# Performance work log

Measured on AMD Instinct MI355X. Metric: run time of the kernel, lower is better.

The kernel has to match this reference:

```python
import jax, jax.numpy as jnp
import numpy as np

N_NODES = 50000
N_EDGES = 100000
NUM_GRAPHS = 1024
EMB = 600
NUM_ATOMIC = 119      # Num_atomic_number
NUM_HYB = 8           # HybridizationType values
NUM_AROM = 2
NUM_CHIR = 4          # ChiralType values
NUM_CHARGE = 9
NUM_BOND_TYPE = 22    # BondType values


def setup_inputs() -> dict:
    key = jax.random.key(0)
    ks = jax.random.split(key, 20)
    # integer graph data
    atom = jnp.stack([
        jax.random.randint(ks[0], (N_NODES,), 0, NUM_ATOMIC),
        jax.random.randint(ks[1], (N_NODES,), 0, NUM_HYB),
        jax.random.randint(ks[2], (N_NODES,), 0, NUM_AROM),
        jax.random.randint(ks[3], (N_NODES,), 0, NUM_CHIR),
        jax.random.randint(ks[4], (N_NODES,), 0, NUM_CHARGE),
    ], axis=1)
    bond_index = jax.random.randint(ks[5], (2, N_EDGES), 0, N_NODES)
    bond_attr = jnp.stack([
        jax.random.randint(ks[6], (N_EDGES,), 0, NUM_BOND_TYPE),
        jax.random.randint(ks[7], (N_EDGES,), 0, NUM_ATOMIC),
    ], axis=1)
    batch = jnp.sort(jax.random.randint(ks[8], (N_NODES,), 0, NUM_GRAPHS))
    # parameters (kaiming-uniform-ish scale)
    def emb(k, n, d):
        bound = float(np.sqrt(6.0 / d))
        return jax.random.uniform(k, (n, d), minval=-bound, maxval=bound, dtype=jnp.float32)
    def lin(k, out_d, in_d):
        bound = float(np.sqrt(6.0 / in_d))
        return jax.random.uniform(k, (out_d, in_d), minval=-bound, maxval=bound, dtype=jnp.float32)
    return {
        "atom": atom, "bond_index": bond_index, "bond_attr": bond_attr, "batch": batch,
        "W_atom_num": emb(ks[9], NUM_ATOMIC, EMB),
        "W_hyb": emb(ks[10], NUM_HYB, EMB),
        "W_arom": emb(ks[11], NUM_AROM, EMB),
        "W_chir": emb(ks[12], NUM_CHIR, EMB),
        "W_charge": emb(ks[13], NUM_CHARGE, EMB),
        "W_bond_type": emb(ks[14], NUM_BOND_TYPE, EMB),
        "W_bond_atom_i": emb(ks[15], NUM_ATOMIC, EMB),
        "W_sl_atom": emb(ks[16], NUM_ATOMIC, EMB),
        "W_sl": emb(ks[17], 1, EMB),
        "W1": lin(ks[18], EMB, EMB), "b1": jnp.zeros((EMB,), jnp.float32),
        "W2": lin(ks[19], EMB // 2, EMB), "b2": jnp.zeros((EMB // 2,), jnp.float32),
        "W3": lin(jax.random.fold_in(key, 99), 1, EMB // 2),
    }


def reference(atom, bond_index, bond_attr, batch,
              W_atom_num, W_hyb, W_arom, W_chir, W_charge,
              W_bond_type, W_bond_atom_i, W_sl_atom, W_sl,
              W1, b1, W2, b2, W3):
    N = atom.shape[0]
    # Step 1: node embedding = sum of 5 lookups  [N, EMB]
    node = (W_atom_num[atom[:, 0]] + W_hyb[atom[:, 1]] + W_arom[atom[:, 2]]
            + W_chir[atom[:, 3]] + W_charge[atom[:, 4]])
    # Step 2: edge embeddings; self-loops appended after real bonds
    bond_emb = W_bond_type[bond_attr[:, 0]] + W_bond_atom_i[bond_attr[:, 1]]  # [E, EMB]
    sl_emb = W_sl_atom[atom[:, 0]] + W_sl[0]                                  # [N, EMB]
    edge_emb = jnp.concatenate([bond_emb, sl_emb], axis=0)                    # [E+N, EMB]
    loop = jnp.arange(N, dtype=bond_index.dtype)
    src = jnp.concatenate([bond_index[0], loop])
    dst = jnp.concatenate([bond_index[1], loop])
    # Step 3: 2 message-passing layers: gather src, multiply edge_emb, scatter-add to dst
    for _ in range(2):
        node = jax.ops.segment_sum(node[src] * edge_emb, dst, num_segments=N)
    # Step 4: energy MLP  ReLU -> Linear(d,d) -> ReLU -> Linear(d,d/2) -> ReLU -> Linear(d/2,1)
    h = jax.nn.relu(node)
    h = jax.nn.relu(h @ W1.T + b1)
    h = jax.nn.relu(h @ W2.T + b2)
    node_energy = h @ W3.T  # [N, 1]
    # Step 5: global add pool per graph
    dg = jax.ops.segment_sum(node_energy, batch, num_segments=NUM_GRAPHS)  # [NUM_GRAPHS, 1]
    return dg
```

## Files before the change

kernel.cpp:

```cpp
#include <hip/hip_runtime.h>

#define EMB 600
#define Q4  150
#define KP  608

typedef unsigned short ushortT;
typedef __attribute__((ext_vector_type(8))) short short8;
typedef __attribute__((ext_vector_type(4))) short short4v;
typedef __attribute__((ext_vector_type(4))) float f32x4;

__device__ __forceinline__ float4 f4add(float4 a, float4 b) {
    return make_float4(a.x + b.x, a.y + b.y, a.z + b.z, a.w + b.w);
}
__device__ __forceinline__ float4 f4fma(float4 acc, float4 v, float4 e) {
    return make_float4(fmaf(v.x, e.x, acc.x), fmaf(v.y, e.y, acc.y),
                       fmaf(v.z, e.z, acc.z), fmaf(v.w, e.w, acc.w));
}
__device__ __forceinline__ ushortT bf16_rne(float x) {
    unsigned u = __float_as_uint(x);
    return (ushortT)((u + 0x7fffu + ((u >> 16) & 1u)) >> 16);
}
__device__ __forceinline__ float bf16_to_f(ushortT h) {
    return __uint_as_float(((unsigned)h) << 16);
}
__device__ __forceinline__ short4v f4_to_bf4(float4 v) {
    short4v r;
    r[0] = (short)bf16_rne(v.x);
    r[1] = (short)bf16_rne(v.y);
    r[2] = (short)bf16_rne(v.z);
    r[3] = (short)bf16_rne(v.w);
    return r;
}
__device__ __forceinline__ float4 bf4_to_f4(short4v h) {
    return make_float4(bf16_to_f((ushortT)h[0]), bf16_to_f((ushortT)h[1]),
                       bf16_to_f((ushortT)h[2]), bf16_to_f((ushortT)h[3]));
}

__device__ __forceinline__ size_t frag_off(int row, int col) {
    return ((size_t)((row >> 4) * 19 + (col >> 5)) * 64
            + (row & 15) + 16 * ((col >> 3) & 3)) * 8 + (col & 7);
}

__global__ void k_node_embed(const int* __restrict__ atom,
                             const float4* __restrict__ Wa,
                             const float4* __restrict__ Wh,
                             const float4* __restrict__ War,
                             const float4* __restrict__ Wc,
                             const float4* __restrict__ Wch,
                             float4* __restrict__ out, int N) {
    int idx = blockIdx.x * blockDim.x + threadIdx.x;
    int total = N * Q4;
    if (idx >= total) return;
    int n = idx / Q4;
    int q = idx - n * Q4;
    const int* a = atom + n * 5;
    float4 r = Wa[a[0] * Q4 + q];
    r = f4add(r, Wh [a[1] * Q4 + q]);
    r = f4add(r, War[a[2] * Q4 + q]);
    r = f4add(r, Wc [a[3] * Q4 + q]);
    r = f4add(r, Wch[a[4] * Q4 + q]);
    out[idx] = r;
}

__global__ void k_hist(const int* __restrict__ bdst, int* __restrict__ counts, int E) {
    int i = blockIdx.x * blockDim.x + threadIdx.x;
    if (i < E) atomicAdd(&counts[bdst[i]], 1);
}

__global__ __launch_bounds__(256) void k_scan_l1(const int* __restrict__ counts,
                                                 int* __restrict__ offsets,
                                                 int* __restrict__ blocksums, int N) {
    __shared__ int s[256];
    int t = threadIdx.x;
    int i = blockIdx.x * 256 + t;
    int v = (i < N) ? counts[i] : 0;
    s[t] = v;
    __syncthreads();
#pragma unroll
    for (int off = 1; off < 256; off <<= 1) {
        int x = (t >= off) ? s[t - off] : 0;
        __syncthreads();
        s[t] += x;
        __syncthreads();
    }
    if (i < N) offsets[i] = s[t] - v;
    if (t == 255) blocksums[blockIdx.x] = s[255];
}

__global__ __launch_bounds__(256) void k_scan_l2(int* __restrict__ blocksums,
                                                 int* __restrict__ blockpref, int nb) {
    __shared__ int s[256];
    int t = threadIdx.x;
    int v = (t < nb) ? blocksums[t] : 0;
    s[t] = v;
    __syncthreads();
#pragma unroll
    for (int off = 1; off < 256; off <<= 1) {
        int x = (t >= off) ? s[t - off] : 0;
        __syncthreads();
        s[t] += x;
        __syncthreads();
    }
    if (t < nb) blockpref[t] = s[t] - v;
}

__global__ __launch_bounds__(256) void k_scan_l3(int* __restrict__ offsets,
                                                 int* __restrict__ cursor,
                                                 const int* __restrict__ blockpref, int N) {
    int i = blockIdx.x * 256 + threadIdx.x;
    if (i < N) {
        int o = offsets[i] + blockpref[blockIdx.x];
        offsets[i] = o;
        cursor[i]  = o;
    }
}

__global__ void k_scatter(const int* __restrict__ bdst, int* __restrict__ cursor,
                          int* __restrict__ edge_list, int E) {
    int i = blockIdx.x * blockDim.x + threadIdx.x;
    if (i < E) {
        int pos = atomicAdd(&cursor[bdst[i]], 1);
        edge_list[pos] = i;
    }
}

__global__ __launch_bounds__(256) void k_mp_gather_b(
        const int* __restrict__ bsrc, const int* __restrict__ battr,
        const int* __restrict__ atom,
        const int* __restrict__ offsets, const int* __restrict__ counts,
        const int* __restrict__ edge_list,
        const float4* __restrict__ Wbt, const float4* __restrict__ Wbai,
        const float4* __restrict__ Wsla, const float4* __restrict__ Wsl,
        const float4* __restrict__ in, ushortT* __restrict__ out, int N) {
    int wid  = (int)((blockIdx.x * blockDim.x + threadIdx.x) >> 6);
    int lane = threadIdx.x & 63;
    int d    = wid >> 1;
    int half = wid & 1;
    if (d >= N) return;
    int q1 = 75 * half + lane;
    int q2 = q1 + 64;
    bool has2 = lane < 11;

    int start = offsets[d], cnt = counts[d];
    int s = 0, t0 = 0, t1 = 0;
    if (cnt > 0) {
        int eid = edge_list[start];
        s  = bsrc[eid];
        t0 = battr[eid * 2 + 0];
        t1 = battr[eid * 2 + 1];
    }

    const float4* slA = Wsla + atom[d * 5] * Q4;
    const float4* inr = in + (size_t)d * Q4;
    float4 acc1 = make_float4(0, 0, 0, 0), acc2 = acc1;
    acc1 = f4fma(acc1, inr[q1], f4add(slA[q1], Wsl[q1]));
    if (has2) acc2 = f4fma(acc2, inr[q2], f4add(slA[q2], Wsl[q2]));

    for (int k = 0; k < cnt; k++) {
        int ns = s, nt0 = t0, nt1 = t1;
        if (k + 1 < cnt) {
            int ne = edge_list[start + k + 1];
            ns  = bsrc[ne];
            nt0 = battr[ne * 2 + 0];
            nt1 = battr[ne * 2 + 1];
        }
        const float4* e0 = Wbt  + t0 * Q4;
        const float4* e1 = Wbai + t1 * Q4;
        const float4* sr = in + (size_t)s * Q4;
        acc1 = f4fma(acc1, sr[q1], f4add(e0[q1], e1[q1]));
        if (has2) acc2 = f4fma(acc2, sr[q2], f4add(e0[q2], e1[q2]));
        s = ns; t0 = nt0; t1 = nt1;
    }
    ushortT* orow = out + (size_t)d * EMB;
    *(short4v*)(orow + q1 * 4) = f4_to_bf4(acc1);
    if (has2) *(short4v*)(orow + q2 * 4) = f4_to_bf4(acc2);
}

__device__ __forceinline__ void frag_store4h(ushortT* __restrict__ hi,
                                             int d, int q, float4 v) {
    int kc = q >> 3, ks = (q >> 1) & 3, halfw = q & 1;
    size_t off = ((size_t)((d >> 4) * 19 + kc) * 64 + (d & 15) + 16 * ks) * 8
                 + halfw * 4;
    float vv[4] = {v.x, v.y, v.z, v.w};
    short4v h4;
#pragma unroll
    for (int j = 0; j < 4; j++)
        h4[j] = (short)bf16_rne(fmaxf(vv[j], 0.f));
    *(short4v*)(hi + off) = h4;
}

__global__ __launch_bounds__(256) void k_mp_gather_rs(
        const int* __restrict__ bsrc, const int* __restrict__ battr,
        const int* __restrict__ atom,
        const int* __restrict__ offsets, const int* __restrict__ counts,
        const int* __restrict__ edge_list,
        const float4* __restrict__ Wbt, const float4* __restrict__ Wbai,
        const float4* __restrict__ Wsla, const float4* __restrict__ Wsl,
        const ushortT* __restrict__ in,
        ushortT* __restrict__ hi, int N) {
    int wid  = (int)((blockIdx.x * blockDim.x + threadIdx.x) >> 6);
    int lane = threadIdx.x & 63;
    int d    = wid >> 1;
    int half = wid & 1;
    if (d >= N) return;
    int q1 = 75 * half + lane;
    int q2 = q1 + 64;
    bool has2 = lane < 11;

    int start = offsets[d], cnt = counts[d];
    int s = 0, t0 = 0, t1 = 0;
    if (cnt > 0) {
        int eid = edge_list[start];
        s  = bsrc[eid];
        t0 = battr[eid * 2 + 0];
        t1 = battr[eid * 2 + 1];
    }

    const float4* slA = Wsla + atom[d * 5] * Q4;
    const ushortT* inr = in + (size_t)d * EMB;
    float4 acc1 = make_float4(0, 0, 0, 0), acc2 = acc1;
    acc1 = f4fma(acc1, bf4_to_f4(*(const short4v*)(inr + q1 * 4)),
                 f4add(slA[q1], Wsl[q1]));
    if (has2) acc2 = f4fma(acc2, bf4_to_f4(*(const short4v*)(inr + q2 * 4)),
                           f4add(slA[q2], Wsl[q2]));

    for (int k = 0; k < cnt; k++) {
        int ns = s, nt0 = t0, nt1 = t1;
        if (k + 1 < cnt) {
            int ne = edge_list[start + k + 1];
            ns  = bsrc[ne];
            nt0 = battr[ne * 2 + 0];
            nt1 = battr[ne * 2 + 1];
        }
        const float4* e0 = Wbt  + t0 * Q4;
        const float4* e1 = Wbai + t1 * Q4;
        const ushortT* sr = in + (size_t)s * EMB;
        acc1 = f4fma(acc1, bf4_to_f4(*(const short4v*)(sr + q1 * 4)),
                     f4add(e0[q1], e1[q1]));
        if (has2) acc2 = f4fma(acc2, bf4_to_f4(*(const short4v*)(sr + q2 * 4)),
                               f4add(e0[q2], e1[q2]));
        s = ns; t0 = nt0; t1 = nt1;
    }
    frag_store4h(hi, d, q1, acc1);
    if (has2) frag_store4h(hi, d, q2, acc2);
    if (half == 0 && lane == 31) {
        size_t off = ((size_t)((d >> 4) * 19 + 18) * 64 + (d & 15) + 48) * 8;
        short8 z = {0, 0, 0, 0, 0, 0, 0, 0};
        *(short8*)(hi + off) = z;
    }
}

__global__ void k_split_w_frag(const float* __restrict__ src,
                               short8* __restrict__ dst,
                               int rows_in, int cb_count) {
    int idx = blockIdx.x * blockDim.x + threadIdx.x;
    int total = cb_count * 19 * 64;
    if (idx >= total) return;
    int lane = idx & 63;
    int tile = idx >> 6;
    int cb = tile / 19, kc = tile - cb * 19;
    int col = cb * 16 + (lane & 15);
    int k0  = kc * 32 + (lane >> 4) * 8;
    short8 h;
#pragma unroll
    for (int j = 0; j < 8; j++) {
        int k = k0 + j;
        float x = (col < rows_in && k < 600) ? src[(size_t)col * 600 + k] : 0.f;
        h[j] = (short)bf16_rne(x);
    }
    dst[idx] = h;
}

struct FragSet { short8 a[4], b[4]; };

__device__ __forceinline__ void frag_load(FragSet& f,
        const short8* __restrict__ Af, const short8* __restrict__ Bf,
        int aBase, int bBase, int kc) {
    int ak = aBase + kc * 64;
    int bk = bBase + kc * 64;
#pragma unroll
    for (int i = 0; i < 4; i++) {
        f.a[i] = Af[ak + i * 1216];
        f.b[i] = Bf[bk + i * 1216];
    }
}

__device__ __forceinline__ void frag_mfma(const FragSet& f, f32x4 acc[4][4]) {
#pragma unroll
    for (int i = 0; i < 4; i++)
#pragma unroll
        for (int j = 0; j < 4; j++)
            acc[i][j] = __builtin_amdgcn_mfma_f32_16x16x32_bf16(f.a[i], f.b[j], acc[i][j], 0, 0, 0);
}

__device__ __forceinline__ void gemm_core_reg(
        const short8* __restrict__ Af, const short8* __restrict__ Bf,
        int aBase, int bBase, f32x4 acc[4][4]) {
    for (int kc = 0; kc < 19; kc++) {
        FragSet f;
        frag_load(f, Af, Bf, aBase, bBase, kc);
        frag_mfma(f, acc);
    }
}

__device__ __forceinline__ void decode_wg(int ncb, int& rowblk, int& colblk) {
    int nwg  = gridDim.x;
    int orig = blockIdx.x;
    int q = nwg >> 3, r = nwg & 7;
    int xcd = orig & 7, rank = orig >> 3;
    int wgid = (xcd < r ? xcd * (q + 1) : r * (q + 1) + (xcd - r) * q) + rank;
    rowblk = wgid / ncb;
    colblk = wgid - rowblk * ncb;
}

__global__ __launch_bounds__(256, 4) void k_gemm1r(
        const short8* __restrict__ Af, const short8* __restrict__ Wf,
        const float* __restrict__ b1,
        ushortT* __restrict__ Hf, int N) {
    int rowblk, colblk;
    decode_wg(5, rowblk, colblk);
    int row0 = rowblk * 128;
    int col0 = colblk * 128;
    int t = threadIdx.x, w = t >> 6, l = t & 63;
    int wr = w >> 1, wc = w & 1, fr = l & 15, fq = l >> 4;

    int aBase = (rowblk * 8 + wr * 4) * 1216 + l;
    int bBase = (colblk * 8 + wc * 4) * 1216 + l;
    f32x4 acc[4][4];
#pragma unroll
    for (int i = 0; i < 4; i++)
#pragma unroll
        for (int j = 0; j < 4; j++) acc[i][j] = f32x4{0.f, 0.f, 0.f, 0.f};
    gemm_core_reg(Af, Wf, aBase, bBase, acc);

#pragma unroll
    for (int i = 0; i < 4; i++) {
#pragma unroll
        for (int j = 0; j < 4; j++) {
            int col = col0 + wc * 64 + j * 16 + fr;
            float bias = (col < 600) ? b1[col] : 0.f;
#pragma unroll
            for (int r = 0; r < 4; r++) {
                int row = row0 + wr * 64 + i * 16 + fq * 4 + r;
                if (row >= N) continue;
                if (col < 600) {
                    float x = fmaxf(acc[i][j][r] + bias, 0.f);
                    Hf[frag_off(row, col)] = bf16_rne(x);
                } else if (col < KP) {
                    Hf[frag_off(row, col)] = 0;
                }
            }
        }
    }
}

__global__ __launch_bounds__(256, 4) void k_gemm2r(
        const short8* __restrict__ Af, const short8* __restrict__ Wf,
        const float* __restrict__ b2, const float* __restrict__ W3,
        float* __restrict__ energy, int N) {
    __shared__ float sE[128];
    int rowblk, colblk;
    decode_wg(3, rowblk, colblk);
    int row0 = rowblk * 128;
    int col0 = colblk * 128;
    int t = threadIdx.x, w = t >> 6, l = t & 63;
    int wr = w >> 1, wc = w & 1, fr = l & 15, fq = l >> 4;

    int aBase = (rowblk * 8 + wr * 4) * 1216 + l;
    int bBase = (colblk * 8 + wc * 4) * 1216 + l;
    f32x4 acc[4][4];
#pragma unroll
    for (int i = 0; i < 4; i++)
#pragma unroll
        for (int j = 0; j < 4; j++) acc[i][j] = f32x4{0.f, 0.f, 0.f, 0.f};
    gemm_core_reg(Af, Wf, aBase, bBase, acc);

    if (t < 128) sE[t] = 0.f;
    __syncthreads();
#pragma unroll
    for (int i = 0; i < 4; i++) {
        float p[4] = {0.f, 0.f, 0.f, 0.f};
#pragma unroll
        for (int j = 0; j < 4; j++) {
            int col = col0 + wc * 64 + j * 16 + fr;
            if (col < 300) {
                float bias = b2[col];
                float wv   = W3[col];
#pragma unroll
                for (int r = 0; r < 4; r++)
                    p[r] += fmaxf(acc[i][j][r] + bias, 0.f) * wv;
            }
        }
#pragma unroll
        for (int r = 0; r < 4; r++) {
            float v = p[r];
            v += __shfl_xor(v, 1, 64);
            v += __shfl_xor(v, 2, 64);
            v += __shfl_xor(v, 4, 64);
            v += __shfl_xor(v, 8, 64);
            p[r] = v;
        }
        if (fr == 0) {
#pragma unroll
            for (int r = 0; r < 4; r++)
                atomicAdd(&sE[wr * 64 + i * 16 + fq * 4 + r], p[r]);
        }
    }
    __syncthreads();
    if (t < 128) {
        int row = row0 + t;
        if (row < N) atomicAdd(&energy[row], sE[t]);
    }
}

__global__ void k_pool(const float* __restrict__ energy, const int* __restrict__ batch,
                       float* __restrict__ dg, int N) {
    int i = blockIdx.x * blockDim.x + threadIdx.x;
    int lane = threadIdx.x & 63;
    float v = (i < N) ? energy[i] : 0.f;
    int   b = (i < N) ? batch[i]  : -1;
#pragma unroll
    for (int off = 1; off < 64; off <<= 1) {
        float vv = __shfl_down(v, off, 64);
        int   bb = __shfl_down(b, off, 64);
        if (lane + off < 64 && bb == b) v += vv;
    }
    int pb = __shfl_up(b, 1, 64);
    if (i < N && (lane == 0 || pb != b)) atomicAdd(&dg[b], v);
}

extern "C" void kernel_launch(void* const* d_in, const int* in_sizes, int n_in,
                              void* d_out, int out_size, void* d_ws, size_t ws_size,
                              hipStream_t stream) {
    const int* atom       = (const int*)d_in[0];
    const int* bond_index = (const int*)d_in[1];
    const int* bond_attr  = (const int*)d_in[2];
    const int* batch      = (const int*)d_in[3];
    const float* Wa   = (const float*)d_in[4];
    const float* Wh   = (const float*)d_in[5];
    const float* War  = (const float*)d_in[6];
    const float* Wc   = (const float*)d_in[7];
    const float* Wch  = (const float*)d_in[8];
    const float* Wbt  = (const float*)d_in[9];
    const float* Wbai = (const float*)d_in[10];
    const float* Wsla = (const float*)d_in[11];
    const float* Wsl  = (const float*)d_in[12];
    const float* W1   = (const float*)d_in[13];
    const float* b1   = (const float*)d_in[14];
    const float* W2   = (const float*)d_in[15];
    const float* b2   = (const float*)d_in[16];
    const float* W3   = (const float*)d_in[17];

    int N = in_sizes[0] / 5;
    int E = in_sizes[1] / 2;
    int Mb = (N + 127) / 128;
    int Npad = Mb * 128;
    int nTiles = Npad / 16;
    int nb = (N + 255) / 256;

    size_t regionBytes = (size_t)Npad * KP * 4;
    char* base = (char*)d_ws;
    float* nodeA = (float*)base;
    ushortT* nodeBh = (ushortT*)(base + regionBytes);
    short8* Af = (short8*)nodeA;
    short8* Hf = (short8*)nodeBh;
    char* tail = base + 2 * regionBytes;
    float* energy  = (float*)tail;
    int* counts    = (int*)(energy + N);
    int* offsets   = counts + N;
    int* cursor    = offsets + N;
    int* edge_list = cursor + N;
    short8* W1f    = (short8*)(edge_list + E);
    short8* W2f    = W1f + 40 * 19 * 64;
    int* blocksums = (int*)(W2f + 24 * 19 * 64);
    int* blockpref = blocksums + 256;

    const int* bsrc = bond_index;
    const int* bdst = bond_index + E;

    hipMemsetAsync(counts, 0, (size_t)N * sizeof(int), stream);
    k_hist<<<(E + 255) / 256, 256, 0, stream>>>(bdst, counts, E);
    k_scan_l1<<<nb, 256, 0, stream>>>(counts, offsets, blocksums, N);
    k_scan_l2<<<1, 256, 0, stream>>>(blocksums, blockpref, nb);
    k_scan_l3<<<nb, 256, 0, stream>>>(offsets, cursor, blockpref, N);
    k_scatter<<<(E + 255) / 256, 256, 0, stream>>>(bdst, cursor, edge_list, E);

    k_split_w_frag<<<(40 * 19 * 64 + 255) / 256, 256, 0, stream>>>(W1, W1f, 600, 40);
    k_split_w_frag<<<(24 * 19 * 64 + 255) / 256, 256, 0, stream>>>(W2, W2f, 300, 24);

    {
        int total = N * Q4;
        k_node_embed<<<(total + 255) / 256, 256, 0, stream>>>(
            atom, (const float4*)Wa, (const float4*)Wh, (const float4*)War,
            (const float4*)Wc, (const float4*)Wch, (float4*)nodeA, N);
    }

    int mpblocks = (2 * N * 64 + 255) / 256;
    k_mp_gather_b<<<mpblocks, 256, 0, stream>>>(bsrc, bond_attr, atom,
        offsets, counts, edge_list,
        (const float4*)Wbt, (const float4*)Wbai, (const float4*)Wsla, (const float4*)Wsl,
        (const float4*)nodeA, nodeBh, N);

    {
        int firstPad = N / 16;
        size_t offB  = (size_t)firstPad * 1216 * 16;
        size_t cntB  = (size_t)(nTiles - firstPad) * 1216 * 16;
        if (cntB) hipMemsetAsync((char*)Af + offB, 0, cntB, stream);
    }

    k_mp_gather_rs<<<mpblocks, 256, 0, stream>>>(bsrc, bond_attr, atom,
        offsets, counts, edge_list,
        (const float4*)Wbt, (const float4*)Wbai, (const float4*)Wsla, (const float4*)Wsl,
        nodeBh, (ushortT*)Af, N);

    k_gemm1r<<<Mb * 5, 256, 0, stream>>>(Af, W1f, b1, (ushortT*)Hf, N);

    hipMemsetAsync(energy, 0, (size_t)N * sizeof(float), stream);
    k_gemm2r<<<Mb * 3, 256, 0, stream>>>(Hf, W2f, b2, W3, energy, N);

    hipMemsetAsync(d_out, 0, (size_t)out_size * sizeof(float), stream);
    k_pool<<<(N + 255) / 256, 256, 0, stream>>>(energy, batch, (float*)d_out, N);
}
```

Before: 348.9 us.

## Store initial node embeddings as bf16 and double-buffer edge gathers in message passing

The initial node embedding is now written in bf16 rather than fp32, which halves the bytes written by the embed kernel and read by the first message-passing layer. Both message-passing kernels share a new loop that fetches the source row and edge weights one edge ahead and the edge indices two edges ahead, so memory latency overlaps with the FMA work. The price is extra registers per thread and bf16 rounding of the layer-1 input, which slightly changes numerics.

Result: slower. 358.2 us (+2.7%).

```diff
diff --git a/kernel.cpp b/kernel.cpp
--- a/kernel.cpp
+++ b/kernel.cpp
@@ -41,13 +41,13 @@
             + (row & 15) + 16 * ((col >> 3) & 3)) * 8 + (col & 7);
 }
 
-__global__ void k_node_embed(const int* __restrict__ atom,
-                             const float4* __restrict__ Wa,
-                             const float4* __restrict__ Wh,
-                             const float4* __restrict__ War,
-                             const float4* __restrict__ Wc,
-                             const float4* __restrict__ Wch,
-                             float4* __restrict__ out, int N) {
+__global__ void k_node_embed_b(const int* __restrict__ atom,
+                               const float4* __restrict__ Wa,
+                               const float4* __restrict__ Wh,
+                               const float4* __restrict__ War,
+                               const float4* __restrict__ Wc,
+                               const float4* __restrict__ Wch,
+                               ushortT* __restrict__ out, int N) {
     int idx = blockIdx.x * blockDim.x + threadIdx.x;
     int total = N * Q4;
     if (idx >= total) return;
@@ -59,7 +59,7 @@
     r = f4add(r, War[a[2] * Q4 + q]);
     r = f4add(r, Wc [a[3] * Q4 + q]);
     r = f4add(r, Wch[a[4] * Q4 + q]);
-    out[idx] = r;
+    *(short4v*)(out + (size_t)n * EMB + q * 4) = f4_to_bf4(r);
 }
 
 __global__ void k_hist(const int* __restrict__ bdst, int* __restrict__ counts, int E) {
@@ -124,6 +124,53 @@
     }
 }
 
+#define MP_PROLOG                                                              \
+    int start = offsets[d], cnt = counts[d];                                   \
+    int s0 = 0, t00 = 0, t01 = 0, s1 = 0, t10 = 0, t11 = 0;                    \
+    if (cnt > 0) {                                                             \
+        int e = edge_list[start];                                              \
+        s0 = bsrc[e]; t00 = battr[2 * e]; t01 = battr[2 * e + 1];              \
+    }                                                                          \
+    if (cnt > 1) {                                                             \
+        int e = edge_list[start + 1];                                          \
+        s1 = bsrc[e]; t10 = battr[2 * e]; t11 = battr[2 * e + 1];              \
+    }                                                                          \
+    short4v cs1 = {0,0,0,0}, cs2 = {0,0,0,0};                                  \
+    float4 ca1 = {}, cb1 = {}, ca2 = {}, cb2 = {};                             \
+    if (cnt > 0) {                                                             \
+        const float4* e0 = Wbt  + t00 * Q4;                                    \
+        const float4* e1 = Wbai + t01 * Q4;                                    \
+        const ushortT* sr = in + (size_t)s0 * EMB;                             \
+        cs1 = *(const short4v*)(sr + q1 * 4);                                  \
+        ca1 = e0[q1]; cb1 = e1[q1];                                            \
+        if (has2) { cs2 = *(const short4v*)(sr + q2 * 4);                      \
+                    ca2 = e0[q2]; cb2 = e1[q2]; }                              \
+    }
+
+#define MP_LOOP                                                                \
+    for (int k = 0; k < cnt; k++) {                                            \
+        short4v xs1 = cs1, xs2 = cs2;                                          \
+        float4 xa1 = ca1, xb1 = cb1, xa2 = ca2, xb2 = cb2;                     \
+        int ms = s1, mt0 = t10, mt1 = t11;                                     \
+        if (k + 2 < cnt) {                                                     \
+            int e = edge_list[start + k + 2];                                  \
+            s1 = bsrc[e]; t10 = battr[2 * e]; t11 = battr[2 * e + 1];          \
+        }                                                                      \
+        if (k + 1 < cnt) {                                                     \
+            const float4* e0 = Wbt  + mt0 * Q4;                                \
+            const float4* e1 = Wbai + mt1 * Q4;                                \
+            const ushortT* sr = in + (size_t)ms * EMB;                         \
+            xs1 = *(const short4v*)(sr + q1 * 4);                              \
+            xa1 = e0[q1]; xb1 = e1[q1];                                        \
+            if (has2) { xs2 = *(const short4v*)(sr + q2 * 4);                  \
+                        xa2 = e0[q2]; xb2 = e1[q2]; }                          \
+        }                                                                      \
+        acc1 = f4fma(acc1, bf4_to_f4(cs1), f4add(ca1, cb1));                   \
+        if (has2) acc2 = f4fma(acc2, bf4_to_f4(cs2), f4add(ca2, cb2));         \
+        cs1 = xs1; ca1 = xa1; cb1 = xb1;                                       \
+        cs2 = xs2; ca2 = xa2; cb2 = xb2;                                       \
+    }
+
 __global__ __launch_bounds__(256) void k_mp_gather_b(
         const int* __restrict__ bsrc, const int* __restrict__ battr,
         const int* __restrict__ atom,
@@ -131,7 +178,7 @@
         const int* __restrict__ edge_list,
         const float4* __restrict__ Wbt, const float4* __restrict__ Wbai,
         const float4* __restrict__ Wsla, const float4* __restrict__ Wsl,
-        const float4* __restrict__ in, ushortT* __restrict__ out, int N) {
+        const ushortT* __restrict__ in, ushortT* __restrict__ out, int N) {
     int wid  = (int)((blockIdx.x * blockDim.x + threadIdx.x) >> 6);
     int lane = threadIdx.x & 63;
     int d    = wid >> 1;
@@ -141,36 +188,18 @@
     int q2 = q1 + 64;
     bool has2 = lane < 11;
 
-    int start = offsets[d], cnt = counts[d];
-    int s = 0, t0 = 0, t1 = 0;
-    if (cnt > 0) {
-        int eid = edge_list[start];
-        s  = bsrc[eid];
-        t0 = battr[eid * 2 + 0];
-        t1 = battr[eid * 2 + 1];
-    }
+    MP_PROLOG
 
     const float4* slA = Wsla + atom[d * 5] * Q4;
-    const float4* inr = in + (size_t)d * Q4;
+    const ushortT* inr = in + (size_t)d * EMB;
     float4 acc1 = make_float4(0, 0, 0, 0), acc2 = acc1;
-    acc1 = f4fma(acc1, inr[q1], f4add(slA[q1], Wsl[q1]));
-    if (has2) acc2 = f4fma(acc2, inr[q2], f4add(slA[q2], Wsl[q2]));
-
-    for (int k = 0; k < cnt; k++) {
-        int ns = s, nt0 = t0, nt1 = t1;
-        if (k + 1 < cnt) {
-            int ne = edge_list[start + k + 1];
-            ns  = bsrc[ne];
-            nt0 = battr[ne * 2 + 0];
-            nt1 = battr[ne * 2 + 1];
-        }
-        const float4* e0 = Wbt  + t0 * Q4;
-        const float4* e1 = Wbai + t1 * Q4;
-        const float4* sr = in + (size_t)s * Q4;
-        acc1 = f4fma(acc1, sr[q1], f4add(e0[q1], e1[q1]));
-        if (has2) acc2 = f4fma(acc2, sr[q2], f4add(e0[q2], e1[q2]));
-        s = ns; t0 = nt0; t1 = nt1;
-    }
+    acc1 = f4fma(acc1, bf4_to_f4(*(const short4v*)(inr + q1 * 4)),
+                 f4add(slA[q1], Wsl[q1]));
+    if (has2) acc2 = f4fma(acc2, bf4_to_f4(*(const short4v*)(inr + q2 * 4)),
+                           f4add(slA[q2], Wsl[q2]));
+
+    MP_LOOP
+
     ushortT* orow = out + (size_t)d * EMB;
     *(short4v*)(orow + q1 * 4) = f4_to_bf4(acc1);
     if (has2) *(short4v*)(orow + q2 * 4) = f4_to_bf4(acc2);
@@ -207,14 +236,7 @@
     int q2 = q1 + 64;
     bool has2 = lane < 11;
 
-    int start = offsets[d], cnt = counts[d];
-    int s = 0, t0 = 0, t1 = 0;
-    if (cnt > 0) {
-        int eid = edge_list[start];
-        s  = bsrc[eid];
-        t0 = battr[eid * 2 + 0];
-        t1 = battr[eid * 2 + 1];
-    }
+    MP_PROLOG
 
     const float4* slA = Wsla + atom[d * 5] * Q4;
     const ushortT* inr = in + (size_t)d * EMB;
@@ -224,23 +246,8 @@
     if (has2) acc2 = f4fma(acc2, bf4_to_f4(*(const short4v*)(inr + q2 * 4)),
                            f4add(slA[q2], Wsl[q2]));
 
-    for (int k = 0; k < cnt; k++) {
-        int ns = s, nt0 = t0, nt1 = t1;
-        if (k + 1 < cnt) {
-            int ne = edge_list[start + k + 1];
-            ns  = bsrc[ne];
-            nt0 = battr[ne * 2 + 0];
-            nt1 = battr[ne * 2 + 1];
-        }
-        const float4* e0 = Wbt  + t0 * Q4;
-        const float4* e1 = Wbai + t1 * Q4;
-        const ushortT* sr = in + (size_t)s * EMB;
-        acc1 = f4fma(acc1, bf4_to_f4(*(const short4v*)(sr + q1 * 4)),
-                     f4add(e0[q1], e1[q1]));
-        if (has2) acc2 = f4fma(acc2, bf4_to_f4(*(const short4v*)(sr + q2 * 4)),
-                               f4add(e0[q2], e1[q2]));
-        s = ns; t0 = nt0; t1 = nt1;
-    }
+    MP_LOOP
+
     frag_store4h(hi, d, q1, acc1);
     if (has2) frag_store4h(hi, d, q2, acc2);
     if (half == 0 && lane == 31) {
@@ -460,9 +467,9 @@
 
     size_t regionBytes = (size_t)Npad * KP * 4;
     char* base = (char*)d_ws;
-    float* nodeA = (float*)base;
+    ushortT* nodeAb = (ushortT*)base;
     ushortT* nodeBh = (ushortT*)(base + regionBytes);
-    short8* Af = (short8*)nodeA;
+    short8* Af = (short8*)nodeAb;
     short8* Hf = (short8*)nodeBh;
     char* tail = base + 2 * regionBytes;
     float* energy  = (float*)tail;
@@ -490,16 +497,16 @@
 
     {
         int total = N * Q4;
-        k_node_embed<<<(total + 255) / 256, 256, 0, stream>>>(
+        k_node_embed_b<<<(total + 255) / 256, 256, 0, stream>>>(
             atom, (const float4*)Wa, (const float4*)Wh, (const float4*)War,
-            (const float4*)Wc, (const float4*)Wch, (float4*)nodeA, N);
+            (const float4*)Wc, (const float4*)Wch, nodeAb, N);
     }
 
     int mpblocks = (2 * N * 64 + 255) / 256;
     k_mp_gather_b<<<mpblocks, 256, 0, stream>>>(bsrc, bond_attr, atom,
         offsets, counts, edge_list,
         (const float4*)Wbt, (const float4*)Wbai, (const float4*)Wsla, (const float4*)Wsl,
-        (const float4*)nodeA, nodeBh, N);
+        nodeAb, nodeBh, N);
 
     {
         int firstPad = N / 16;
```
